# Optimization experiments

Measured on AMD Instinct MI355X. Metric: run time of the kernel, lower is better.

## Reference

```python
import jax, jax.numpy as jnp
import numpy as np

N, E, D, H, C = 100000, 1600000, 64, 8, 10
NEG_SLOPE = 0.2


def setup_inputs() -> dict:
    key = jax.random.key(0)
    ks = jax.random.split(key, 20)
    rn = lambda k, sh: jax.random.normal(k, sh, jnp.float32) * 0.1
    return dict(
        x=jax.random.normal(ks[0], (N, D), jnp.float32),
        edge_index=jax.random.randint(ks[1], (2, E), 0, N),
        gcnK_W=rn(ks[2], (D, D)), gcnK_b=rn(ks[3], (D,)),
        gcnV_W=rn(ks[4], (D, D)), gcnV_b=rn(ks[5], (D,)),
        super_Q=rn(ks[6], (C, D)),
        mha_in_w=rn(ks[7], (3 * D, D)), mha_in_b=rn(ks[8], (3 * D,)),
        mha_out_w=rn(ks[9], (D, D)), mha_out_b=rn(ks[10], (D,)),
        gat_W=rn(ks[11], (D, D)), gat_Wc=rn(ks[12], (D, D)),
        gat_a_src=rn(ks[13], (D,)), gat_a_dst=rn(ks[14], (D,)),
        gat_b=rn(ks[15], (D,)),
        t1_W=rn(ks[16], (D, 2 * D)), t1_b=rn(ks[17], (2 * D,)),
        t2_W=rn(ks[18], (2 * D, D)), t2_b=rn(ks[19], (D,)),
    )


def _gcn(x, W, b, src, dst, norm_e):
    # PyG GCNConv: symmetric-normalized aggregation over (A + I)
    h = x @ W  # [N, D]
    agg = jax.ops.segment_sum(h[src] * norm_e[:, None], dst, num_segments=N)
    return agg + b


def _mha(q, k, v, in_w, in_b, out_w, out_b):
    # torch.nn.MultiheadAttention (unbatched), eval mode (dropout off)
    L, n, hd = q.shape[0], k.shape[0], D // H
    Wq, Wk, Wv = jnp.split(in_w, 3, axis=0)
    bq, bk, bv = jnp.split(in_b, 3)
    scale = 1.0 / float(np.sqrt(hd))
    qh = ((q @ Wq.T + bq) * scale).reshape(L, H, hd).transpose(1, 0, 2)  # [H,L,hd]
    kh = (k @ Wk.T + bk).reshape(n, H, hd).transpose(1, 0, 2)            # [H,n,hd]
    vh = (v @ Wv.T + bv).reshape(n, H, hd).transpose(1, 0, 2)
    attn = jax.nn.softmax(jnp.einsum('hld,hnd->hln', qh, kh), axis=-1)
    o = jnp.einsum('hln,hnd->hld', attn, vh).transpose(1, 0, 2).reshape(L, D)
    return o @ out_w.T + out_b


def _context_gat(x, src, dst, context, W, Wc, a_src, a_dst, b):
    # context-conditioned GAT: per-edge logits use node terms + global context gate
    h = x @ W
    c = context @ Wc  # [D]
    s_src = h @ (a_src + c)  # context modulates source attention vector
    s_dst = h @ a_dst
    logits = jax.nn.leaky_relu(s_src[src] + s_dst[dst], NEG_SLOPE)  # [E]
    m = jax.ops.segment_max(logits, dst, num_segments=N)
    ex = jnp.exp(logits - m[dst])
    denom = jax.ops.segment_sum(ex, dst, num_segments=N)
    alpha = ex / (denom[dst] + 1e-16)
    out = jax.ops.segment_sum(alpha[:, None] * h[src], dst, num_segments=N)
    return out + b


def reference(x, edge_index, gcnK_W, gcnK_b, gcnV_W, gcnV_b, super_Q,
              mha_in_w, mha_in_b, mha_out_w, mha_out_b,
              gat_W, gat_Wc, gat_a_src, gat_a_dst, gat_b,
              t1_W, t1_b, t2_W, t2_b):
    src, dst = edge_index[0], edge_index[1]
    loop = jnp.arange(N)
    srcl = jnp.concatenate([src, loop])
    dstl = jnp.concatenate([dst, loop])
    deg = jax.ops.segment_sum(jnp.ones_like(srcl, jnp.float32), dstl, num_segments=N)
    dinv = jnp.where(deg > 0, 1.0 / jnp.sqrt(deg), 0.0)
    norm_e = dinv[srcl] * dinv[dstl]
    x_K = _gcn(x, gcnK_W, gcnK_b, srcl, dstl, norm_e)
    x_V = _gcn(x, gcnV_W, gcnV_b, srcl, dstl, norm_e)
    cluster = _mha(super_Q, x_K, x_V, mha_in_w, mha_in_b, mha_out_w, mha_out_b)  # [C, D]
    context = jnp.mean(cluster, axis=0)  # [D]
    g = _context_gat(x_V, src, dst, context, gat_W, gat_Wc, gat_a_src, gat_a_dst, gat_b)
    h1 = jax.nn.relu(g @ t1_W + t1_b)
    return jax.nn.relu(h1 @ t2_W + t2_b)
```

## Files before the change

### kernel.cpp

```cpp
#include <hip/hip_runtime.h>
#include <hip/hip_bf16.h>
#include <stdint.h>

#define NN 100000
#define EE 1600000
#define NBK 391
#define CHUNK 4096
#define NCB 98
#define NPROJ 1563
#define NS 32

#define FMA4(xi, vv, a, base)                      \
  a[(base)+0] = fmaf((xi), (vv).x, a[(base)+0]);   \
  a[(base)+1] = fmaf((xi), (vv).y, a[(base)+1]);   \
  a[(base)+2] = fmaf((xi), (vv).z, a[(base)+2]);   \
  a[(base)+3] = fmaf((xi), (vv).w, a[(base)+3]);

typedef __attribute__((ext_vector_type(8))) short bf16x8;
typedef __attribute__((ext_vector_type(4))) float f32x4;
typedef __attribute__((ext_vector_type(2))) float f32x2;
union FragU { uint4 u; bf16x8 h; };

__device__ inline unsigned pack_bf2(float a, float b) {
  __hip_bfloat162 t;
  t.x = __float2bfloat16(a);
  t.y = __float2bfloat16(b);
  return *reinterpret_cast<unsigned*>(&t);
}

__device__ inline f32x2 unpk2(unsigned u) {
  f32x2 r;
  r.x = __uint_as_float(u << 16);
  r.y = __uint_as_float(u & 0xffff0000u);
  return r;
}

__launch_bounds__(256)
__global__ void k_hist(const int* __restrict__ ei, int* __restrict__ histmat) {
  __shared__ int hist[NCB];
  int t = threadIdx.x;
  if (t < NCB) hist[t] = 0;
  __syncthreads();
  int base = blockIdx.x * CHUNK;
  int nb = EE - base; if (nb > CHUNK) nb = CHUNK;
  for (int k = t; k < nb; k += 256)
    atomicAdd(&hist[ei[EE + base + k] >> 10], 1);
  __syncthreads();
  if (t < NCB) histmat[blockIdx.x * NCB + t] = hist[t];
}

__launch_bounds__(256)
__global__ void k_sumcb(const int* __restrict__ histmat, int* __restrict__ cbsum) {
  __shared__ int red[4];
  int cb = blockIdx.x, t = threadIdx.x;
  int s = 0;
  for (int blk = t; blk < NBK; blk += 256) s += histmat[blk * NCB + cb];
#pragma unroll
  for (int off = 32; off > 0; off >>= 1) s += __shfl_down(s, off);
  if ((t & 63) == 0) red[t >> 6] = s;
  __syncthreads();
  if (t == 0) cbsum[cb] = red[0] + red[1] + red[2] + red[3];
}

__launch_bounds__(512)
__global__ void k_ppos(const int* __restrict__ histmat, const int* __restrict__ cbsum,
                       int* __restrict__ bstart, int* __restrict__ offsets,
                       int* __restrict__ ppos) {
  __shared__ int sm[512];
  __shared__ int sb[128];
  int cb = blockIdx.x, t = threadIdx.x;
  if (t < 128) sb[t] = (t < NCB) ? cbsum[t] : 0;
  __syncthreads();
  for (int off = 1; off < 128; off <<= 1) {
    int x = (t < 128 && t >= off) ? sb[t - off] : 0;
    __syncthreads();
    if (t < 128) sb[t] += x;
    __syncthreads();
  }
  int bs = (cb == 0) ? 0 : sb[cb - 1];
  if (t == 0) bstart[cb] = bs;
  if (cb == 0 && t == 0) { bstart[NCB] = EE; offsets[NN] = EE; }
  int v = (t < NBK) ? histmat[t * NCB + cb] : 0;
  sm[t] = v;
  __syncthreads();
  for (int off = 1; off < 512; off <<= 1) {
    int x = (t >= off) ? sm[t - off] : 0;
    __syncthreads();
    sm[t] += x;
    __syncthreads();
  }
  if (t < NBK) ppos[cb * NBK + t] = bs + sm[t] - v;
}

__launch_bounds__(256)
__global__ void k_fill_b(const int* __restrict__ ei, const int* __restrict__ ppos,
                         unsigned* __restrict__ brec) {
  __shared__ int hist[NCB], binstart[NCB], bincur[NCB], pbase[NCB];
  __shared__ unsigned lbuf[CHUNK];
  __shared__ unsigned char cbArr[CHUNK];
  int t = threadIdx.x;
  int base = blockIdx.x * CHUNK;
  int nb = EE - base; if (nb > CHUNK) nb = CHUNK;
  if (t < NCB) { hist[t] = 0; pbase[t] = ppos[t * NBK + blockIdx.x]; }
  __syncthreads();
  unsigned rec[16]; int rcb[16]; int cnt = 0;
  for (int k = t; k < nb; k += 256) {
    int s = ei[base + k], d = ei[EE + base + k];
    rec[cnt] = (unsigned)s | ((unsigned)(d & 1023) << 17);
    rcb[cnt] = d >> 10;
    atomicAdd(&hist[rcb[cnt]], 1);
    cnt++;
  }
  __syncthreads();
  if (t < NCB) binstart[t] = hist[t];
  __syncthreads();
  for (int off = 1; off < NCB; off <<= 1) {
    int v = (t < NCB && t >= off) ? binstart[t - off] : 0;
    __syncthreads();
    if (t < NCB) binstart[t] += v;
    __syncthreads();
  }
  if (t < NCB) { binstart[t] -= hist[t]; bincur[t] = 0; }
  __syncthreads();
  for (int i = 0; i < cnt; i++) {
    int c = rcb[i];
    int pos = atomicAdd(&bincur[c], 1);
    int p = binstart[c] + pos;
    lbuf[p] = rec[i];
    cbArr[p] = (unsigned char)c;
  }
  __syncthreads();
  for (int i = t; i < nb; i += 256) {
    int c = cbArr[i];
    brec[pbase[c] + (i - binstart[c])] = lbuf[i];
  }
}

__launch_bounds__(1024)
__global__ void k_fill_c(const unsigned* __restrict__ brec, const int* __restrict__ bstart,
                         int* __restrict__ csr, int* __restrict__ offsets,
                         float* __restrict__ dinv) {
  __shared__ int cnt[1024], sm[1024];
  int cbk = blockIdx.x, t = threadIdx.x;
  int nb0 = cbk << 10;
  int nn = NN - nb0; if (nn > 1024) nn = 1024;
  cnt[t] = 0;
  __syncthreads();
  int e0 = bstart[cbk], e1 = bstart[cbk + 1];
  for (int j = e0 + t; j < e1; j += 1024)
    atomicAdd(&cnt[brec[j] >> 17], 1);
  __syncthreads();
  int cv = cnt[t];
  sm[t] = cv;
  __syncthreads();
  for (int off = 1; off < 1024; off <<= 1) {
    int v = (t >= off) ? sm[t - off] : 0;
    __syncthreads();
    sm[t] += v;
    __syncthreads();
  }
  sm[t] -= cv;
  if (t < nn) {
    offsets[nb0 + t] = e0 + sm[t];
    dinv[nb0 + t] = rsqrtf((float)(cv + 1));
  }
  cnt[t] = 0;
  __syncthreads();
  for (int j = e0 + t; j < e1; j += 1024) {
    unsigned r = brec[j];
    int dl = r >> 17;
    int p = atomicAdd(&cnt[dl], 1);
    csr[e0 + sm[dl] + p] = r & 0x1FFFF;
  }
}

__global__ void k_prep(const float* __restrict__ x, const float* __restrict__ dinv,
                       unsigned* __restrict__ xbf2) {
  int i = blockIdx.x * 256 + threadIdx.x;
  if (i >= NN * 32) return;
  float dv = dinv[i >> 5];
  float2 v = ((const float2*)x)[i];
  xbf2[i] = pack_bf2(v.x * dv, v.y * dv);
}

__launch_bounds__(256)
__global__ void k_agg_x(const unsigned* __restrict__ xbf2, const int* __restrict__ offsets,
                        const int* __restrict__ csr, const float* __restrict__ dinv,
                        unsigned* __restrict__ axb) {
  int gid = blockIdx.x * 256 + threadIdx.x;
  int n = gid >> 6;
  if (n >= NN) return;
  int lane = gid & 63, q = lane & 7, grp = lane >> 3;
  int e0 = offsets[n], e1 = offsets[n + 1];
  float dv = dinv[n];
  f32x2 a2[4];
#pragma unroll
  for (int i = 0; i < 4; i++) a2[i] = (f32x2){0.f, 0.f};
  if (grp == 0) {
    uint4 u = ((const uint4*)(xbf2 + (size_t)n * 32))[q];
    unsigned uu[4] = {u.x, u.y, u.z, u.w};
#pragma unroll
    for (int p = 0; p < 4; p++) a2[p] += unpk2(uu[p]);
  }
  int b2 = e0;
  for (; b2 + 8 < e1; b2 += 16) {
    int j0 = b2 + grp, j1 = j0 + 8;
    int s0 = csr[j0];
    bool ok1 = j1 < e1;
    int s1 = ok1 ? csr[j1] : s0;
    uint4 u0 = ((const uint4*)(xbf2 + (size_t)s0 * 32))[q];
    uint4 u1 = ((const uint4*)(xbf2 + (size_t)s1 * 32))[q];
    unsigned w0[4] = {u0.x, u0.y, u0.z, u0.w};
    unsigned w1[4] = {u1.x, u1.y, u1.z, u1.w};
#pragma unroll
    for (int p = 0; p < 4; p++) a2[p] += unpk2(w0[p]);
    if (ok1) {
#pragma unroll
      for (int p = 0; p < 4; p++) a2[p] += unpk2(w1[p]);
    }
  }
  for (; b2 < e1; b2 += 8) {
    int j = b2 + grp;
    if (j < e1) {
      int s = csr[j];
      uint4 u = ((const uint4*)(xbf2 + (size_t)s * 32))[q];
      unsigned uu[4] = {u.x, u.y, u.z, u.w};
#pragma unroll
      for (int p = 0; p < 4; p++) a2[p] += unpk2(uu[p]);
    }
  }
#pragma unroll
  for (int i = 0; i < 4; i++) {
    a2[i].x += __shfl_xor(a2[i].x, 8);
    a2[i].x += __shfl_xor(a2[i].x, 16);
    a2[i].x += __shfl_xor(a2[i].x, 32);
    a2[i].y += __shfl_xor(a2[i].y, 8);
    a2[i].y += __shfl_xor(a2[i].y, 16);
    a2[i].y += __shfl_xor(a2[i].y, 32);
  }
  if (lane < 8) {
    uint4 u;
    u.x = pack_bf2(a2[0].x * dv, a2[0].y * dv);
    u.y = pack_bf2(a2[1].x * dv, a2[1].y * dv);
    u.z = pack_bf2(a2[2].x * dv, a2[2].y * dv);
    u.w = pack_bf2(a2[3].x * dv, a2[3].y * dv);
    ((uint4*)(axb + (size_t)n * 32))[q] = u;
  }
}

__launch_bounds__(256)
__global__ void k_fusew(const float* __restrict__ gcnK_W, const float* __restrict__ gcnK_b,
                        const float* __restrict__ gcnV_W, const float* __restrict__ gcnV_b,
                        const float* __restrict__ mha_in_w, const float* __restrict__ mha_in_b,
                        const float* __restrict__ gat_W, const float* __restrict__ sQ,
                        unsigned* __restrict__ Wt, float* __restrict__ bb) {
  __shared__ float sW1[64 * 65];
  __shared__ float sW2[64 * 65];
  __shared__ float sW3[64 * 65];
  __shared__ float sqq[640], qhs[640], Ms[5120], kb[64];
  int blk = blockIdx.x, t = threadIdx.x;
  const float scale = 0.35355339059327373f;
  if (blk < 16) {
    for (int i = t; i < 4096; i += 256) sW1[(i >> 6) * 65 + (i & 63)] = gcnV_W[i];
    if (blk < 8) {
      for (int i = t; i < 512; i += 256) sW2[i] = mha_in_w[(128 + blk * 8) * 64 + i];
    } else {
      for (int i = t; i < 4096; i += 256) sW2[(i >> 6) * 65 + (i & 63)] = gat_W[i];
    }
    __syncthreads();
    int idx = blk * 256 + t;
    int d = idx >> 5, kp = idx & 31;
    float v2[2];
#pragma unroll
    for (int u2 = 0; u2 < 2; u2++) {
      int k = kp * 2 + u2;
      float s = 0.f;
      if (d < 64) {
        int r = d & 7;
        for (int j = 0; j < 64; j++) s = fmaf(sW1[k * 65 + j], sW2[r * 64 + j], s);
      } else {
        int c = d - 64;
        for (int j = 0; j < 64; j++) s = fmaf(sW1[k * 65 + j], sW2[j * 65 + c], s);
      }
      v2[u2] = s;
    }
    Wt[idx] = pack_bf2(v2[0], v2[1]);
    if (t < 8) {
      if (blk < 8) {
        int d0 = blk * 8 + t;
        float s = mha_in_b[128 + d0];
        for (int j = 0; j < 64; j++) s = fmaf(gcnV_b[j], sW2[t * 64 + j], s);
        bb[d0] = s;
      } else {
        int c = (blk - 8) * 8 + t;
        float s = 0.f;
        for (int j = 0; j < 64; j++) s = fmaf(gcnV_b[j], sW2[j * 65 + c], s);
        bb[64 + c] = s;
      }
    }
  } else {
    for (int i = t; i < 4096; i += 256) {
      int r = i >> 6, c = i & 63;
      sW1[r * 65 + c] = gcnK_W[i];
      sW2[r * 65 + c] = mha_in_w[64 * 64 + i];
      sW3[r * 65 + c] = mha_in_w[i];
    }
    for (int i = t; i < 640; i += 256) sqq[i] = sQ[i];
    __syncthreads();
    for (int e = t; e < 640; e += 256) {
      int lv = e >> 6, c = e & 63;
      float acc = mha_in_b[c];
      for (int i = 0; i < 64; i++) acc = fmaf(sqq[lv * 64 + i], sW3[c * 65 + i], acc);
      qhs[e] = acc * scale;
    }
    if (t < 64) {
      float s = mha_in_b[64 + t];
      for (int j = 0; j < 64; j++) s = fmaf(gcnK_b[j], sW2[t * 65 + j], s);
      kb[t] = s;
    }
    __syncthreads();
    for (int e = t; e < 5120; e += 256) {
      int j = e / 80, hl = e % 80;
      int h = hl / 10, lv = hl % 10;
      float s = 0.f;
#pragma unroll
      for (int c = 0; c < 8; c++) {
        int cp = h * 8 + c;
        s = fmaf(sW2[cp * 65 + j], qhs[lv * 64 + cp], s);
      }
      Ms[j * 80 + hl] = s;
    }
    if (t < 80) {
      int h = t / 10, lv = t % 10;
      float s = 0.f;
#pragma unroll
      for (int c = 0; c < 8; c++) {
        int cp = h * 8 + c;
        s = fmaf(kb[cp], qhs[lv * 64 + cp], s);
      }
      bb[128 + t] = s;
    }
    __syncthreads();
    for (int e = t; e < 2560; e += 256) {
      int hl = e >> 5, kp = e & 31;
      float v2[2];
#pragma unroll
      for (int u2 = 0; u2 < 2; u2++) {
        int k = kp * 2 + u2;
        float s = 0.f;
        for (int j = 0; j < 64; j++) s = fmaf(sW1[k * 65 + j], Ms[j * 80 + hl], s);
        v2[u2] = s;
      }
      Wt[(128 + hl) * 32 + kp] = pack_bf2(v2[0], v2[1]);
    }
  }
}

__launch_bounds__(256)
__global__ void k_proj(const unsigned* __restrict__ axb, const unsigned* __restrict__ Wt,
                       const float* __restrict__ bb, const float* __restrict__ a_dst,
                       unsigned* __restrict__ hGb, unsigned char* __restrict__ hG8,
                       float* __restrict__ s_dstv, float* __restrict__ part2) {
  __shared__ float red[4][720];
  int t = threadIdx.x;
  int wid = t >> 6, l = t & 63;
  int l15 = l & 15, lg = l >> 4;
  int base = blockIdx.x * 64;
  int rowbase = base + wid * 16;

  FragU a0, a1;
  {
    int r = rowbase + l15;
    if (r < NN) {
      const uint4* p = (const uint4*)(axb + (size_t)r * 32);
      a0.u = p[lg];
      a1.u = p[4 + lg];
    } else {
      a0.u = make_uint4(0u, 0u, 0u, 0u);
      a1.u = a0.u;
    }
  }
  f32x4 acc[13];
#pragma unroll
  for (int ct = 0; ct < 13; ct++) acc[ct] = (f32x4){0.f, 0.f, 0.f, 0.f};
#pragma unroll
  for (int ct = 0; ct < 13; ct++) {
    const uint4* wp = (const uint4*)(Wt + (size_t)(ct * 16 + l15) * 32);
    FragU b0, b1;
    b0.u = wp[lg];
    b1.u = wp[4 + lg];
    acc[ct] = __builtin_amdgcn_mfma_f32_16x16x32_bf16(a0.h, b0.h, acc[ct], 0, 0, 0);
    acc[ct] = __builtin_amdgcn_mfma_f32_16x16x32_bf16(a1.h, b1.h, acc[ct], 0, 0, 0);
  }

  float sdp[4] = {0.f, 0.f, 0.f, 0.f};
  __hip_bfloat16* hgp = (__hip_bfloat16*)hGb;
#pragma unroll
  for (int gt = 0; gt < 4; gt++) {
    int col = gt * 16 + l15;
    float bias = bb[64 + col];
    float ad = a_dst[col];
#pragma unroll
    for (int r = 0; r < 4; r++) {
      float hg = acc[4 + gt][r] + bias;
      sdp[r] = fmaf(hg, ad, sdp[r]);
      int row = rowbase + lg * 4 + r;
      if (row < NN) {
        hgp[(size_t)row * 64 + col] = __float2bfloat16(hg);
        unsigned wq = __builtin_amdgcn_cvt_pk_fp8_f32(hg, hg, 0u, false);
        hG8[(size_t)row * 64 + col] = (unsigned char)(wq & 0xffu);
      }
    }
  }
#pragma unroll
  for (int r = 0; r < 4; r++) {
    float v = sdp[r];
    v += __shfl_xor(v, 1); v += __shfl_xor(v, 2);
    v += __shfl_xor(v, 4); v += __shfl_xor(v, 8);
    int row = rowbase + lg * 4 + r;
    if (l15 == 0 && row < NN) s_dstv[row] = v;
  }

  float wz[5][4];
#pragma unroll
  for (int zt = 0; zt < 5; zt++) {
    int zcol = zt * 16 + l15;
    float bias = bb[128 + zcol];
    float sp = 0.f;
#pragma unroll
    for (int r = 0; r < 4; r++) {
      int row = rowbase + lg * 4 + r;
      float z = acc[8 + zt][r] + bias;
      float w = (row < NN) ? __expf(z) : 0.f;
      wz[zt][r] = w;
      sp += w;
    }
    sp += __shfl_xor(sp, 16);
    sp += __shfl_xor(sp, 32);
    if (l < 16) {
      int h = zcol / 10, lv = zcol % 10;
      red[wid][h * 90 + lv] = sp;
    }
  }

  int sA = (l15 + 32 * lg) & 63;
  int sB2 = (sA + 16) & 63;
  bool loK = (lg < 2);
  FragU af[5];
#pragma unroll
  for (int zt = 0; zt < 5; zt++) {
    unsigned wlo = pack_bf2(wz[zt][0], wz[zt][1]);
    unsigned whi = pack_bf2(wz[zt][2], wz[zt][3]);
    unsigned f0 = __shfl(wlo, sA), f1 = __shfl(whi, sA);
    unsigned f2 = __shfl(wlo, sB2), f3 = __shfl(whi, sB2);
    af[zt].u.x = loK ? f0 : 0u;
    af[zt].u.y = loK ? f1 : 0u;
    af[zt].u.z = loK ? f2 : 0u;
    af[zt].u.w = loK ? f3 : 0u;
  }
#pragma unroll
  for (int vt = 0; vt < 4; vt++) {
    float bias = bb[vt * 16 + l15];
    unsigned vlo = pack_bf2(acc[vt][0] + bias, acc[vt][1] + bias);
    unsigned vhi = pack_bf2(acc[vt][2] + bias, acc[vt][3] + bias);
    FragU bf;
    {
      unsigned f0 = __shfl(vlo, sA), f1 = __shfl(vhi, sA);
      unsigned f2 = __shfl(vlo, sB2), f3 = __shfl(vhi, sB2);
      bf.u.x = loK ? f0 : 0u;
      bf.u.y = loK ? f1 : 0u;
      bf.u.z = loK ? f2 : 0u;
      bf.u.w = loK ? f3 : 0u;
    }
    f32x4 oacc[5];
#pragma unroll
    for (int zt = 0; zt < 5; zt++) {
      oacc[zt] = (f32x4){0.f, 0.f, 0.f, 0.f};
      oacc[zt] = __builtin_amdgcn_mfma_f32_16x16x32_bf16(af[zt].h, bf.h, oacc[zt], 0, 0, 0);
    }
#pragma unroll
    for (int zt = 0; zt < 5; zt++) {
#pragma unroll
      for (int r = 0; r < 4; r++) {
        int hl = zt * 16 + lg * 4 + r;
        int h = hl / 10, lv = hl - h * 10;
        if (vt * 2 + (l15 >> 3) == h)
          red[wid][h * 90 + 10 + lv * 8 + (l15 & 7)] = oacc[zt][r];
      }
    }
  }

  __syncthreads();
  float* p2 = part2 + (size_t)(blockIdx.x & (NS - 1)) * 720;
  for (int j = t; j < 720; j += 256) {
    float v = red[0][j] + red[1][j] + red[2][j] + red[3][j];
    atomicAdd(&p2[j], v);
  }
}

__global__ void k_context(const float* __restrict__ part2, const float* __restrict__ out_w,
                          const float* __restrict__ out_b, const float* __restrict__ a_src,
                          const float* __restrict__ gat_Wc, float* __restrict__ aeff) {
  __shared__ float po[640], cl[640], ctx[64], ac[720];
  int t = threadIdx.x;
  for (int j = t; j < 720; j += 640) {
    float v = 0.f;
#pragma unroll
    for (int s = 0; s < NS; s++) v += part2[(size_t)s * 720 + j];
    int cg = j / 90, r = j % 90;
    ac[(r < 10) ? (cg * 10 + r) : (80 + cg * 80 + (r - 10))] = v;
  }
  __syncthreads();
  {
    int h = t / 80, r = t % 80, l = r >> 3, j = r & 7;
    po[l * 64 + h * 8 + j] = ac[80 + t] / ac[h * 10 + l];
  }
  __syncthreads();
  {
    int l = t >> 6, d = t & 63;
    float v = out_b[d];
    for (int c = 0; c < 64; c++) v = fmaf(po[l * 64 + c], out_w[d * 64 + c], v);
    cl[t] = v;
  }
  __syncthreads();
  if (t < 64) {
    float m = 0.f;
#pragma unroll
    for (int l = 0; l < 10; l++) m += cl[l * 64 + t];
    ctx[t] = m * 0.1f;
  }
  __syncthreads();
  if (t < 64) {
    float v = a_src[t];
    for (int i = 0; i < 64; i++) v = fmaf(ctx[i], gat_Wc[i * 64 + t], v);
    aeff[t] = v;
  }
}

__launch_bounds__(256)
__global__ void k_ssrc(const unsigned* __restrict__ hGb, const float* __restrict__ aeff,
                       float* __restrict__ s_src) {
  int gid = blockIdx.x * 256 + threadIdx.x;
  int n = gid >> 6, lane = gid & 63;
  if (n >= NN) return;
  const __hip_bfloat16* hp = (const __hip_bfloat16*)hGb;
  float v = __bfloat162float(hp[(size_t)n * 64 + lane]) * aeff[lane];
#pragma unroll
  for (int off = 32; off > 0; off >>= 1) v += __shfl_xor(v, off);
  if (lane == 0) s_src[n] = v;
}

__launch_bounds__(256)
__global__ void k_gat(const int* __restrict__ offsets, const int* __restrict__ csr,
                      const float* __restrict__ s_src, const float* __restrict__ s_dstv,
                      const unsigned char* __restrict__ hG8, const float* __restrict__ gat_b,
                      unsigned* __restrict__ gb) {
  int gid = blockIdx.x * 256 + threadIdx.x;
  int n = gid >> 6;
  if (n >= NN) return;
  int lane = gid & 63, q = lane & 7, grp = lane >> 3;
  int e0 = offsets[n], e1 = offsets[n + 1];
  float sd = s_dstv[n];
  float den = 0.f;
  f32x2 a2[4];
#pragma unroll
  for (int i = 0; i < 4; i++) a2[i] = (f32x2){0.f, 0.f};
  int b2 = e0;
  for (; b2 + 8 < e1; b2 += 16) {
    int j0 = b2 + grp, j1 = j0 + 8;
    int s0 = csr[j0];
    bool ok1 = j1 < e1;
    int s1 = ok1 ? csr[j1] : s0;
    float z0 = s_src[s0] + sd;
    float z1 = s_src[s1] + sd;
    uint2 u0 = ((const uint2*)(hG8 + (size_t)s0 * 64))[q];
    uint2 u1 = ((const uint2*)(hG8 + (size_t)s1 * 64))[q];
    z0 = z0 > 0.f ? z0 : 0.2f * z0;
    float ex0 = __expf(z0);
    den += ex0;
    f32x2 e0v = (f32x2){ex0, ex0};
    {
      f32x2 p0 = __builtin_amdgcn_cvt_pk_f32_fp8(u0.x, false);
      f32x2 p1 = __builtin_amdgcn_cvt_pk_f32_fp8(u0.x, true);
      f32x2 p2 = __builtin_amdgcn_cvt_pk_f32_fp8(u0.y, false);
      f32x2 p3 = __builtin_amdgcn_cvt_pk_f32_fp8(u0.y, true);
      a2[0] = e0v * p0 + a2[0];
      a2[1] = e0v * p1 + a2[1];
      a2[2] = e0v * p2 + a2[2];
      a2[3] = e0v * p3 + a2[3];
    }
    if (ok1) {
      z1 = z1 > 0.f ? z1 : 0.2f * z1;
      float ex1 = __expf(z1);
      den += ex1;
      f32x2 e1v = (f32x2){ex1, ex1};
      f32x2 p0 = __builtin_amdgcn_cvt_pk_f32_fp8(u1.x, false);
      f32x2 p1 = __builtin_amdgcn_cvt_pk_f32_fp8(u1.x, true);
      f32x2 p2 = __builtin_amdgcn_cvt_pk_f32_fp8(u1.y, false);
      f32x2 p3 = __builtin_amdgcn_cvt_pk_f32_fp8(u1.y, true);
      a2[0] = e1v * p0 + a2[0];
      a2[1] = e1v * p1 + a2[1];
      a2[2] = e1v * p2 + a2[2];
      a2[3] = e1v * p3 + a2[3];
    }
  }
  for (; b2 < e1; b2 += 8) {
    int j = b2 + grp;
    if (j < e1) {
      int s = csr[j];
      float z = s_src[s] + sd;
      z = z > 0.f ? z : 0.2f * z;
      float ex = __expf(z);
      den += ex;
      uint2 u = ((const uint2*)(hG8 + (size_t)s * 64))[q];
      f32x2 ev = (f32x2){ex, ex};
      f32x2 p0 = __builtin_amdgcn_cvt_pk_f32_fp8(u.x, false);
      f32x2 p1 = __builtin_amdgcn_cvt_pk_f32_fp8(u.x, true);
      f32x2 p2 = __builtin_amdgcn_cvt_pk_f32_fp8(u.y, false);
      f32x2 p3 = __builtin_amdgcn_cvt_pk_f32_fp8(u.y, true);
      a2[0] = ev * p0 + a2[0];
      a2[1] = ev * p1 + a2[1];
      a2[2] = ev * p2 + a2[2];
      a2[3] = ev * p3 + a2[3];
    }
  }
  den += __shfl_xor(den, 8);
  den += __shfl_xor(den, 16);
  den += __shfl_xor(den, 32);
#pragma unroll
  for (int i = 0; i < 4; i++) {
    a2[i].x += __shfl_xor(a2[i].x, 8);
    a2[i].x += __shfl_xor(a2[i].x, 16);
    a2[i].x += __shfl_xor(a2[i].x, 32);
    a2[i].y += __shfl_xor(a2[i].y, 8);
    a2[i].y += __shfl_xor(a2[i].y, 16);
    a2[i].y += __shfl_xor(a2[i].y, 32);
  }
  float inv = 1.f / (den + 1e-16f);
  if (lane < 8) {
    uint4 u;
    u.x = pack_bf2(a2[0].x * inv + gat_b[q * 8 + 0], a2[0].y * inv + gat_b[q * 8 + 1]);
    u.y = pack_bf2(a2[1].x * inv + gat_b[q * 8 + 2], a2[1].y * inv + gat_b[q * 8 + 3]);
    u.z = pack_bf2(a2[2].x * inv + gat_b[q * 8 + 4], a2[2].y * inv + gat_b[q * 8 + 5]);
    u.w = pack_bf2(a2[3].x * inv + gat_b[q * 8 + 6], a2[3].y * inv + gat_b[q * 8 + 7]);
    ((uint4*)(gb + (size_t)n * 32))[q] = u;
  }
}

__launch_bounds__(256)
__global__ void k_mlp1(const unsigned* __restrict__ gb, const float* __restrict__ W1,
                       const float* __restrict__ b1, unsigned* __restrict__ h1b) {
  __shared__ float sX[32 * 65];
  __shared__ float sW[64 * 128];
  __shared__ float sb[128];
  int t = threadIdx.x;
  int base = blockIdx.x * 32;
  for (int i = t; i < 8192; i += 256) sW[i] = W1[i];
  if (t < 128) sb[t] = b1[t];
  for (int idx = t; idx < 32 * 8; idx += 256) {
    int rl = idx >> 3, c8 = idx & 7;
    int row = base + rl;
    uint4 u = (row < NN) ? ((const uint4*)(gb + (size_t)row * 32))[c8]
                         : make_uint4(0u, 0u, 0u, 0u);
    unsigned uu[4] = {u.x, u.y, u.z, u.w};
    float* dst = sX + rl * 65 + c8 * 8;
#pragma unroll
    for (int p = 0; p < 4; p++) {
      __hip_bfloat162 v = *reinterpret_cast<__hip_bfloat162*>(&uu[p]);
      dst[2 * p] = __bfloat162float(v.x);
      dst[2 * p + 1] = __bfloat162float(v.y);
    }
  }
  __syncthreads();
  int cg = t & 15, rg = t >> 4;
  int r0 = rg * 2;
  float a0[8], a1[8];
#pragma unroll
  for (int i = 0; i < 8; i++) { a0[i] = 0.f; a1[i] = 0.f; }
  const float4* W4 = (const float4*)sW;
#pragma unroll 4
  for (int i = 0; i < 64; i++) {
    float x0 = sX[r0 * 65 + i];
    float x1 = sX[(r0 + 1) * 65 + i];
    float4 w0 = W4[i * 32 + cg * 2], w1 = W4[i * 32 + cg * 2 + 1];
    FMA4(x0, w0, a0, 0); FMA4(x0, w1, a0, 4);
    FMA4(x1, w0, a1, 0); FMA4(x1, w1, a1, 4);
  }
#pragma unroll
  for (int r = 0; r < 2; r++) {
    int row = base + r0 + r;
    if (row >= NN) continue;
    float* a = r ? a1 : a0;
    float h[8];
#pragma unroll
    for (int c = 0; c < 8; c++) h[c] = fmaxf(a[c] + sb[cg * 8 + c], 0.f);
    uint4 u;
    u.x = pack_bf2(h[0], h[1]);
    u.y = pack_bf2(h[2], h[3]);
    u.z = pack_bf2(h[4], h[5]);
    u.w = pack_bf2(h[6], h[7]);
    ((uint4*)(h1b + (size_t)row * 64))[cg] = u;
  }
}

__launch_bounds__(256)
__global__ void k_mlp2(const unsigned* __restrict__ h1b, const float* __restrict__ W2,
                       const float* __restrict__ b2, float* __restrict__ out) {
  __shared__ unsigned sH[64 * 65];
  __shared__ float sW[128 * 64];
  __shared__ float sb[64];
  int t = threadIdx.x;
  int base = blockIdx.x * 64;
  for (int i = t; i < 8192; i += 256) sW[i] = W2[i];
  if (t < 64) sb[t] = b2[t];
  for (int idx = t; idx < 64 * 16; idx += 256) {
    int rl = idx >> 4, c4 = idx & 15;
    int row = base + rl;
    uint4 v = (row < NN) ? ((const uint4*)h1b)[(size_t)row * 16 + c4]
                         : make_uint4(0u, 0u, 0u, 0u);
    sH[rl * 65 + 4 * c4 + 0] = v.x;
    sH[rl * 65 + 4 * c4 + 1] = v.y;
    sH[rl * 65 + 4 * c4 + 2] = v.z;
    sH[rl * 65 + 4 * c4 + 3] = v.w;
  }
  __syncthreads();
  int cg = t & 7, rg = t >> 3;
  int r0 = rg * 2;
  float a0[8], a1[8];
#pragma unroll
  for (int i = 0; i < 8; i++) { a0[i] = 0.f; a1[i] = 0.f; }
  const float4* W4 = (const float4*)sW;
#pragma unroll 2
  for (int kp = 0; kp < 64; kp++) {
    unsigned u0 = sH[r0 * 65 + kp];
    unsigned u1 = sH[(r0 + 1) * 65 + kp];
    float x0a = __uint_as_float(u0 << 16), x0b = __uint_as_float(u0 & 0xffff0000u);
    float x1a = __uint_as_float(u1 << 16), x1b = __uint_as_float(u1 & 0xffff0000u);
    int k0 = 2 * kp, k1 = 2 * kp + 1;
    float4 wa0 = W4[k0 * 16 + cg * 2], wa1 = W4[k0 * 16 + cg * 2 + 1];
    float4 wb0 = W4[k1 * 16 + cg * 2], wb1 = W4[k1 * 16 + cg * 2 + 1];
    FMA4(x0a, wa0, a0, 0); FMA4(x0a, wa1, a0, 4);
    FMA4(x0b, wb0, a0, 0); FMA4(x0b, wb1, a0, 4);
    FMA4(x1a, wa0, a1, 0); FMA4(x1a, wa1, a1, 4);
    FMA4(x1b, wb0, a1, 0); FMA4(x1b, wb1, a1, 4);
  }
#pragma unroll
  for (int r = 0; r < 2; r++) {
    int row = base + r0 + r;
    if (row >= NN) continue;
    float* a = r ? a1 : a0;
    float4* op = (float4*)(out + (size_t)row * 64 + cg * 8);
    op[0] = make_float4(fmaxf(a[0] + sb[cg * 8 + 0], 0.f), fmaxf(a[1] + sb[cg * 8 + 1], 0.f),
                        fmaxf(a[2] + sb[cg * 8 + 2], 0.f), fmaxf(a[3] + sb[cg * 8 + 3], 0.f));
    op[1] = make_float4(fmaxf(a[4] + sb[cg * 8 + 4], 0.f), fmaxf(a[5] + sb[cg * 8 + 5], 0.f),
                        fmaxf(a[6] + sb[cg * 8 + 6], 0.f), fmaxf(a[7] + sb[cg * 8 + 7], 0.f));
  }
}

extern "C" void kernel_launch(void* const* d_in, const int* in_sizes, int n_in,
                              void* d_out, int out_size, void* d_ws, size_t ws_size,
                              hipStream_t stream) {
  (void)in_sizes; (void)n_in; (void)out_size; (void)ws_size;
  const float* x        = (const float*)d_in[0];
  const int*   ei       = (const int*)d_in[1];
  const float* gcnK_W   = (const float*)d_in[2];
  const float* gcnK_b   = (const float*)d_in[3];
  const float* gcnV_W   = (const float*)d_in[4];
  const float* gcnV_b   = (const float*)d_in[5];
  const float* super_Q  = (const float*)d_in[6];
  const float* mha_in_w = (const float*)d_in[7];
  const float* mha_in_b = (const float*)d_in[8];
  const float* mha_out_w= (const float*)d_in[9];
  const float* mha_out_b= (const float*)d_in[10];
  const float* gat_W    = (const float*)d_in[11];
  const float* gat_Wc   = (const float*)d_in[12];
  const float* gat_a_src= (const float*)d_in[13];
  const float* gat_a_dst= (const float*)d_in[14];
  const float* gat_b    = (const float*)d_in[15];
  const float* t1_W     = (const float*)d_in[16];
  const float* t1_b     = (const float*)d_in[17];
  const float* t2_W     = (const float*)d_in[18];
  const float* t2_b     = (const float*)d_in[19];

  char* ws = (char*)d_ws;
  size_t cur = 0;
  auto alloc = [&](size_t bytes) -> char* {
    char* p = ws + cur;
    cur = (cur + bytes + 255) & ~(size_t)255;
    return p;
  };
  int*      histmat = (int*)alloc((size_t)NBK * NCB * 4);
  int*      cbsum   = (int*)alloc((size_t)NCB * 4);
  int*      ppos    = (int*)alloc((size_t)NCB * NBK * 4);
  int*      bstart  = (int*)alloc((size_t)(NCB + 1) * 4);
  int*      offsets = (int*)alloc((size_t)(NN + 1) * 4);
  float*    dinv    = (float*)alloc((size_t)NN * 4);
  int*      csr     = (int*)alloc((size_t)EE * 4);
  unsigned* brec    = (unsigned*)alloc((size_t)EE * 4);
  unsigned* Wt      = (unsigned*)alloc((size_t)208 * 32 * 4);
  float*    bb      = (float*)alloc(208 * 4);
  float*    aeff    = (float*)alloc(64 * 4);
  float*    part2   = (float*)alloc((size_t)NS * 720 * 4);
  float*    s_src   = (float*)alloc((size_t)NN * 4);
  float*    s_dstv  = (float*)alloc((size_t)NN * 4);
  unsigned* xbf     = (unsigned*)alloc((size_t)NN * 128);
  unsigned* axb     = (unsigned*)alloc((size_t)NN * 128);
  unsigned* hGb     = (unsigned*)alloc((size_t)NN * 128);
  unsigned char* hG8 = (unsigned char*)alloc((size_t)NN * 64);
  unsigned* gb      = (unsigned*)alloc((size_t)NN * 128);
  unsigned* h1b     = (unsigned*)alloc((size_t)NN * 64 * 4);
  float*    g       = (float*)d_out;

  hipMemsetAsync(part2, 0, (size_t)NS * 720 * 4, stream);
  k_hist<<<NBK, 256, 0, stream>>>(ei, histmat);
  k_sumcb<<<NCB, 256, 0, stream>>>(histmat, cbsum);
  k_ppos<<<NCB, 512, 0, stream>>>(histmat, cbsum, bstart, offsets, ppos);
  k_fill_b<<<NBK, 256, 0, stream>>>(ei, ppos, brec);
  k_fill_c<<<NCB, 1024, 0, stream>>>(brec, bstart, csr, offsets, dinv);
  k_prep<<<(NN * 32 + 255) / 256, 256, 0, stream>>>(x, dinv, xbf);
  k_agg_x<<<NN / 4, 256, 0, stream>>>(xbf, offsets, csr, dinv, axb);
  k_fusew<<<17, 256, 0, stream>>>(gcnK_W, gcnK_b, gcnV_W, gcnV_b, mha_in_w, mha_in_b,
                                  gat_W, super_Q, Wt, bb);
  k_proj<<<NPROJ, 256, 0, stream>>>(axb, Wt, bb, gat_a_dst, hGb, hG8, s_dstv, part2);
  k_context<<<1, 640, 0, stream>>>(part2, mha_out_w, mha_out_b, gat_a_src, gat_Wc, aeff);
  k_ssrc<<<NN / 4, 256, 0, stream>>>(hGb, aeff, s_src);
  k_gat<<<NN / 4, 256, 0, stream>>>(offsets, csr, s_src, s_dstv, hG8, gat_b, gb);
  k_mlp1<<<(NN + 31) / 32, 256, 0, stream>>>(gb, t1_W, t1_b, h1b);
  k_mlp2<<<(NN + 63) / 64, 256, 0, stream>>>(h1b, t2_W, t2_b, g);
}
```

Measured before the change: 395.3 us.

## Use bf16 MFMA for the two MLP layers with prepacked weights

Both MLP kernels switch from fp32 FMA loops over LDS-staged weights to bf16 16x16x32 MFMA instructions. A-fragments are loaded directly from global memory. The MLP weights are pre-transposed and packed to bf16 once, in extra blocks of the existing weight-fusion kernel. This removes per-block LDS weight staging and the scalar FMA work. In exchange, the weights are now rounded to bf16 and the output stores are scattered per element.

Result: faster. 380.1 us (-3.9%).

```diff
diff --git a/kernel.cpp b/kernel.cpp
--- a/kernel.cpp
+++ b/kernel.cpp
@@ -9,12 +9,6 @@
 #define NCB 98
 #define NPROJ 1563
 #define NS 32
-
-#define FMA4(xi, vv, a, base)                      \
-  a[(base)+0] = fmaf((xi), (vv).x, a[(base)+0]);   \
-  a[(base)+1] = fmaf((xi), (vv).y, a[(base)+1]);   \
-  a[(base)+2] = fmaf((xi), (vv).z, a[(base)+2]);   \
-  a[(base)+3] = fmaf((xi), (vv).w, a[(base)+3]);
 
 typedef __attribute__((ext_vector_type(8))) short bf16x8;
 typedef __attribute__((ext_vector_type(4))) float f32x4;
@@ -253,7 +247,9 @@
                         const float* __restrict__ gcnV_W, const float* __restrict__ gcnV_b,
                         const float* __restrict__ mha_in_w, const float* __restrict__ mha_in_b,
                         const float* __restrict__ gat_W, const float* __restrict__ sQ,
-                        unsigned* __restrict__ Wt, float* __restrict__ bb) {
+                        const float* __restrict__ t1W, const float* __restrict__ t2W,
+                        unsigned* __restrict__ Wt, float* __restrict__ bb,
+                        unsigned* __restrict__ W1b, unsigned* __restrict__ W2b) {
   __shared__ float sW1[64 * 65];
   __shared__ float sW2[64 * 65];
   __shared__ float sW3[64 * 65];
@@ -298,7 +294,7 @@
         bb[64 + c] = s;
       }
     }
-  } else {
+  } else if (blk == 16) {
     for (int i = t; i < 4096; i += 256) {
       int r = i >> 6, c = i & 63;
       sW1[r * 65 + c] = gcnK_W[i];
@@ -353,6 +349,14 @@
       }
       Wt[(128 + hl) * 32 + kp] = pack_bf2(v2[0], v2[1]);
     }
+  } else if (blk < 33) {
+    int idx = (blk - 17) * 256 + t;
+    int col = idx >> 5, kp = idx & 31;
+    W1b[idx] = pack_bf2(t1W[(2 * kp) * 128 + col], t1W[(2 * kp + 1) * 128 + col]);
+  } else {
+    int idx = (blk - 33) * 256 + t;
+    int col = idx >> 6, kp = idx & 63;
+    W2b[idx] = pack_bf2(t2W[(2 * kp) * 64 + col], t2W[(2 * kp + 1) * 64 + col]);
   }
 }
 
@@ -648,112 +652,90 @@
 }
 
 __launch_bounds__(256)
-__global__ void k_mlp1(const unsigned* __restrict__ gb, const float* __restrict__ W1,
+__global__ void k_mlp1(const unsigned* __restrict__ gb, const unsigned* __restrict__ W1b,
                        const float* __restrict__ b1, unsigned* __restrict__ h1b) {
-  __shared__ float sX[32 * 65];
-  __shared__ float sW[64 * 128];
-  __shared__ float sb[128];
   int t = threadIdx.x;
-  int base = blockIdx.x * 32;
-  for (int i = t; i < 8192; i += 256) sW[i] = W1[i];
-  if (t < 128) sb[t] = b1[t];
-  for (int idx = t; idx < 32 * 8; idx += 256) {
-    int rl = idx >> 3, c8 = idx & 7;
-    int row = base + rl;
-    uint4 u = (row < NN) ? ((const uint4*)(gb + (size_t)row * 32))[c8]
-                         : make_uint4(0u, 0u, 0u, 0u);
-    unsigned uu[4] = {u.x, u.y, u.z, u.w};
-    float* dst = sX + rl * 65 + c8 * 8;
-#pragma unroll
-    for (int p = 0; p < 4; p++) {
-      __hip_bfloat162 v = *reinterpret_cast<__hip_bfloat162*>(&uu[p]);
-      dst[2 * p] = __bfloat162float(v.x);
-      dst[2 * p + 1] = __bfloat162float(v.y);
-    }
-  }
-  __syncthreads();
-  int cg = t & 15, rg = t >> 4;
-  int r0 = rg * 2;
-  float a0[8], a1[8];
-#pragma unroll
-  for (int i = 0; i < 8; i++) { a0[i] = 0.f; a1[i] = 0.f; }
-  const float4* W4 = (const float4*)sW;
-#pragma unroll 4
-  for (int i = 0; i < 64; i++) {
-    float x0 = sX[r0 * 65 + i];
-    float x1 = sX[(r0 + 1) * 65 + i];
-    float4 w0 = W4[i * 32 + cg * 2], w1 = W4[i * 32 + cg * 2 + 1];
-    FMA4(x0, w0, a0, 0); FMA4(x0, w1, a0, 4);
-    FMA4(x1, w0, a1, 0); FMA4(x1, w1, a1, 4);
-  }
-#pragma unroll
-  for (int r = 0; r < 2; r++) {
-    int row = base + r0 + r;
-    if (row >= NN) continue;
-    float* a = r ? a1 : a0;
-    float h[8];
-#pragma unroll
-    for (int c = 0; c < 8; c++) h[c] = fmaxf(a[c] + sb[cg * 8 + c], 0.f);
-    uint4 u;
-    u.x = pack_bf2(h[0], h[1]);
-    u.y = pack_bf2(h[2], h[3]);
-    u.z = pack_bf2(h[4], h[5]);
-    u.w = pack_bf2(h[6], h[7]);
-    ((uint4*)(h1b + (size_t)row * 64))[cg] = u;
-  }
-}
-
-__launch_bounds__(256)
-__global__ void k_mlp2(const unsigned* __restrict__ h1b, const float* __restrict__ W2,
+  int wid = t >> 6, l = t & 63;
+  int l15 = l & 15, lg = l >> 4;
+  int rowbase = blockIdx.x * 64 + wid * 16;
+  FragU a0, a1;
+  {
+    int r = rowbase + l15;
+    if (r < NN) {
+      const uint4* p = (const uint4*)(gb + (size_t)r * 32);
+      a0.u = p[lg];
+      a1.u = p[4 + lg];
+    } else {
+      a0.u = make_uint4(0u, 0u, 0u, 0u);
+      a1.u = a0.u;
+    }
+  }
+  f32x4 acc[8];
+#pragma unroll
+  for (int ct = 0; ct < 8; ct++) acc[ct] = (f32x4){0.f, 0.f, 0.f, 0.f};
+#pragma unroll
+  for (int ct = 0; ct < 8; ct++) {
+    const uint4* wp = (const uint4*)(W1b + (size_t)(ct * 16 + l15) * 32);
+    FragU b0, b1f;
+    b0.u = wp[lg];
+    b1f.u = wp[4 + lg];
+    acc[ct] = __builtin_amdgcn_mfma_f32_16x16x32_bf16(a0.h, b0.h, acc[ct], 0, 0, 0);
+    acc[ct] = __builtin_amdgcn_mfma_f32_16x16x32_bf16(a1.h, b1f.h, acc[ct], 0, 0, 0);
+  }
+  __hip_bfloat16* hp = (__hip_bfloat16*)h1b;
+#pragma unroll
+  for (int ct = 0; ct < 8; ct++) {
+    int col = ct * 16 + l15;
+    float bias = b1[col];
+#pragma unroll
+    for (int r = 0; r < 4; r++) {
+      int row = rowbase + lg * 4 + r;
+      if (row < NN) hp[(size_t)row * 128 + col] = __float2bfloat16(fmaxf(acc[ct][r] + bias, 0.f));
+    }
+  }
+}
+
+__launch_bounds__(256)
+__global__ void k_mlp2(const unsigned* __restrict__ h1b, const unsigned* __restrict__ W2b,
                        const float* __restrict__ b2, float* __restrict__ out) {
-  __shared__ unsigned sH[64 * 65];
-  __shared__ float sW[128 * 64];
-  __shared__ float sb[64];
   int t = threadIdx.x;
-  int base = blockIdx.x * 64;
-  for (int i = t; i < 8192; i += 256) sW[i] = W2[i];
-  if (t < 64) sb[t] = b2[t];
-  for (int idx = t; idx < 64 * 16; idx += 256) {
-    int rl = idx >> 4, c4 = idx & 15;
-    int row = base + rl;
-    uint4 v = (row < NN) ? ((const uint4*)h1b)[(size_t)row * 16 + c4]
-                         : make_uint4(0u, 0u, 0u, 0u);
-    sH[rl * 65 + 4 * c4 + 0] = v.x;
-    sH[rl * 65 + 4 * c4 + 1] = v.y;
-    sH[rl * 65 + 4 * c4 + 2] = v.z;
-    sH[rl * 65 + 4 * c4 + 3] = v.w;
-  }
-  __syncthreads();
-  int cg = t & 7, rg = t >> 3;
-  int r0 = rg * 2;
-  float a0[8], a1[8];
-#pragma unroll
-  for (int i = 0; i < 8; i++) { a0[i] = 0.f; a1[i] = 0.f; }
-  const float4* W4 = (const float4*)sW;
-#pragma unroll 2
-  for (int kp = 0; kp < 64; kp++) {
-    unsigned u0 = sH[r0 * 65 + kp];
-    unsigned u1 = sH[(r0 + 1) * 65 + kp];
-    float x0a = __uint_as_float(u0 << 16), x0b = __uint_as_float(u0 & 0xffff0000u);
-    float x1a = __uint_as_float(u1 << 16), x1b = __uint_as_float(u1 & 0xffff0000u);
-    int k0 = 2 * kp, k1 = 2 * kp + 1;
-    float4 wa0 = W4[k0 * 16 + cg * 2], wa1 = W4[k0 * 16 + cg * 2 + 1];
-    float4 wb0 = W4[k1 * 16 + cg * 2], wb1 = W4[k1 * 16 + cg * 2 + 1];
-    FMA4(x0a, wa0, a0, 0); FMA4(x0a, wa1, a0, 4);
-    FMA4(x0b, wb0, a0, 0); FMA4(x0b, wb1, a0, 4);
-    FMA4(x1a, wa0, a1, 0); FMA4(x1a, wa1, a1, 4);
-    FMA4(x1b, wb0, a1, 0); FMA4(x1b, wb1, a1, 4);
-  }
-#pragma unroll
-  for (int r = 0; r < 2; r++) {
-    int row = base + r0 + r;
-    if (row >= NN) continue;
-    float* a = r ? a1 : a0;
-    float4* op = (float4*)(out + (size_t)row * 64 + cg * 8);
-    op[0] = make_float4(fmaxf(a[0] + sb[cg * 8 + 0], 0.f), fmaxf(a[1] + sb[cg * 8 + 1], 0.f),
-                        fmaxf(a[2] + sb[cg * 8 + 2], 0.f), fmaxf(a[3] + sb[cg * 8 + 3], 0.f));
-    op[1] = make_float4(fmaxf(a[4] + sb[cg * 8 + 4], 0.f), fmaxf(a[5] + sb[cg * 8 + 5], 0.f),
-                        fmaxf(a[6] + sb[cg * 8 + 6], 0.f), fmaxf(a[7] + sb[cg * 8 + 7], 0.f));
+  int wid = t >> 6, l = t & 63;
+  int l15 = l & 15, lg = l >> 4;
+  int rowbase = blockIdx.x * 64 + wid * 16;
+  FragU a[4];
+  {
+    int r = rowbase + l15;
+    if (r < NN) {
+      const uint4* p = (const uint4*)(h1b + (size_t)r * 64);
+#pragma unroll
+      for (int ks = 0; ks < 4; ks++) a[ks].u = p[4 * ks + lg];
+    } else {
+#pragma unroll
+      for (int ks = 0; ks < 4; ks++) a[ks].u = make_uint4(0u, 0u, 0u, 0u);
+    }
+  }
+  f32x4 acc[4];
+#pragma unroll
+  for (int ct = 0; ct < 4; ct++) acc[ct] = (f32x4){0.f, 0.f, 0.f, 0.f};
+#pragma unroll
+  for (int ct = 0; ct < 4; ct++) {
+    const uint4* wp = (const uint4*)(W2b + (size_t)(ct * 16 + l15) * 64);
+#pragma unroll
+    for (int ks = 0; ks < 4; ks++) {
+      FragU bf;
+      bf.u = wp[4 * ks + lg];
+      acc[ct] = __builtin_amdgcn_mfma_f32_16x16x32_bf16(a[ks].h, bf.h, acc[ct], 0, 0, 0);
+    }
+  }
+#pragma unroll
+  for (int ct = 0; ct < 4; ct++) {
+    int col = ct * 16 + l15;
+    float bias = b2[col];
+#pragma unroll
+    for (int r = 0; r < 4; r++) {
+      int row = rowbase + lg * 4 + r;
+      if (row < NN) out[(size_t)row * 64 + col] = fmaxf(acc[ct][r] + bias, 0.f);
+    }
   }
 }
 
@@ -799,6 +781,8 @@
   unsigned* brec    = (unsigned*)alloc((size_t)EE * 4);
   unsigned* Wt      = (unsigned*)alloc((size_t)208 * 32 * 4);
   float*    bb      = (float*)alloc(208 * 4);
+  unsigned* W1b     = (unsigned*)alloc((size_t)4096 * 4);
+  unsigned* W2b     = (unsigned*)alloc((size_t)4096 * 4);
   float*    aeff    = (float*)alloc(64 * 4);
   float*    part2   = (float*)alloc((size_t)NS * 720 * 4);
   float*    s_src   = (float*)alloc((size_t)NN * 4);
@@ -819,12 +803,12 @@
   k_fill_c<<<NCB, 1024, 0, stream>>>(brec, bstart, csr, offsets, dinv);
   k_prep<<<(NN * 32 + 255) / 256, 256, 0, stream>>>(x, dinv, xbf);
   k_agg_x<<<NN / 4, 256, 0, stream>>>(xbf, offsets, csr, dinv, axb);
-  k_fusew<<<17, 256, 0, stream>>>(gcnK_W, gcnK_b, gcnV_W, gcnV_b, mha_in_w, mha_in_b,
-                                  gat_W, super_Q, Wt, bb);
+  k_fusew<<<49, 256, 0, stream>>>(gcnK_W, gcnK_b, gcnV_W, gcnV_b, mha_in_w, mha_in_b,
+                                  gat_W, super_Q, t1_W, t2_W, Wt, bb, W1b, W2b);
   k_proj<<<NPROJ, 256, 0, stream>>>(axb, Wt, bb, gat_a_dst, hGb, hG8, s_dstv, part2);
   k_context<<<1, 640, 0, stream>>>(part2, mha_out_w, mha_out_b, gat_a_src, gat_Wc, aeff);
   k_ssrc<<<NN / 4, 256, 0, stream>>>(hGb, aeff, s_src);
   k_gat<<<NN / 4, 256, 0, stream>>>(offsets, csr, s_src, s_dstv, hG8, gat_b, gb);
-  k_mlp1<<<(NN + 31) / 32, 256, 0, stream>>>(gb, t1_W, t1_b, h1b);
-  k_mlp2<<<(NN + 63) / 64, 256, 0, stream>>>(h1b, t2_W, t2_b, g);
-}
+  k_mlp1<<<(NN + 63) / 64, 256, 0, stream>>>(gb, W1b, t1_b, h1b);
+  k_mlp2<<<(NN + 63) / 64, 256, 0, stream>>>(h1b, W2b, t2_b, g);
+}
```
